# Kernel tuning notes

Measured on AMD Instinct MI355X. Metric: run time of the kernel, lower is better.

Reference implementation:

```python
import jax, jax.numpy as jnp
import numpy as np

SEQ = 8192
VOCAB = 100000
EMB = 256
HID = 4            # must equal N_QUBITS for the gate elementwise math to broadcast
N_QUBITS = 4
TAGS = 10


def _qlayer(x, p):
    """Analytic 4-qubit circuit: RX(x_w) then RX(p_w) per wire, CNOT ring, PauliZ expvals.

    Consecutive RX gates add angles: a_w = x_w + p_w; single-qubit <Z> = cos(a_w).
    CNOTs permute computational basis states, so final bit w is an XOR of the
    independent input bits along the ring, giving products of cos terms:
      <Z_0> = z1*z2*z3, <Z_1> = z0*z1, <Z_2> = z0*z1*z2, <Z_3> = z0*z1*z2*z3.
    x: [B, 4], p: [4] -> [B, 4]
    """
    z = jnp.cos(x + p)
    z0, z1, z2, z3 = z[:, 0], z[:, 1], z[:, 2], z[:, 3]
    return jnp.stack([z1 * z2 * z3, z0 * z1, z0 * z1 * z2, z0 * z1 * z2 * z3], axis=-1)


def setup_inputs() -> dict:
    key = jax.random.key(0)
    ks = jax.random.split(key, 16)
    s = 1.0 / np.sqrt(EMB + HID)
    inp = {
        "sentence": jax.random.randint(ks[0], (SEQ,), 0, VOCAB),
        "embed": jax.random.normal(ks[1], (VOCAB, EMB), dtype=jnp.float32),
        "Wf": jax.random.uniform(ks[2], (EMB + HID, N_QUBITS), minval=-s, maxval=s),
        "bf": jax.random.uniform(ks[3], (N_QUBITS,), minval=-s, maxval=s),
        "Wi": jax.random.uniform(ks[4], (EMB + HID, N_QUBITS), minval=-s, maxval=s),
        "bi": jax.random.uniform(ks[5], (N_QUBITS,), minval=-s, maxval=s),
        "Wu": jax.random.uniform(ks[6], (EMB + HID, N_QUBITS), minval=-s, maxval=s),
        "bu": jax.random.uniform(ks[7], (N_QUBITS,), minval=-s, maxval=s),
        "Wo": jax.random.uniform(ks[8], (EMB + HID, N_QUBITS), minval=-s, maxval=s),
        "bo": jax.random.uniform(ks[9], (N_QUBITS,), minval=-s, maxval=s),
        "pf": jax.random.uniform(ks[10], (N_QUBITS,), minval=0.0, maxval=2 * np.pi),
        "pi_": jax.random.uniform(ks[11], (N_QUBITS,), minval=0.0, maxval=2 * np.pi),
        "pu": jax.random.uniform(ks[12], (N_QUBITS,), minval=0.0, maxval=2 * np.pi),
        "po": jax.random.uniform(ks[13], (N_QUBITS,), minval=0.0, maxval=2 * np.pi),
        "W_tag": jax.random.uniform(ks[14], (HID, TAGS), minval=-0.5, maxval=0.5),
        "b_tag": jax.random.uniform(ks[15], (TAGS,), minval=-0.5, maxval=0.5),
    }
    return inp


def reference(sentence, embed, Wf, bf, Wi, bi, Wu, bu, Wo, bo, pf, pi_, pu, po, W_tag, b_tag):
    embeds = embed[sentence]  # [S, EMB] gather (memory-bound)

    def step(carry, x):
        hx, cx = carry  # each [1, HID]
        comb = jnp.concatenate([x[None, :], hx], axis=1)  # [1, EMB+HID]
        f = jax.nn.sigmoid(_qlayer(comb @ Wf + bf, pf))
        i = jax.nn.sigmoid(_qlayer(comb @ Wi + bi, pi_))
        g = jnp.tanh(_qlayer(comb @ Wu + bu, pu))
        o = jax.nn.sigmoid(_qlayer(comb @ Wo + bo, po))
        cx = f * cx + i * g
        hx = o * jnp.tanh(cx)
        return (hx, cx), hx[0]

    init = (jnp.zeros((1, HID), embeds.dtype), jnp.zeros((1, HID), embeds.dtype))
    _, outs = jax.lax.scan(step, init, embeds)  # outs: [S, HID]
    logits = outs @ W_tag + b_tag  # [S, TAGS]
    return jax.nn.log_softmax(logits, axis=1)
```

## Files before the change

### kernel.cpp

```cpp
#include <hip/hip_runtime.h>
#include <hip/hip_bf16.h>

#define SEQ   8192
#define EMB   256
#define TAGS  10
#define PFD   8
#define CHUNK 8
#define WARM  16

static_assert(SEQ % CHUNK == 0, "chunks tile SEQ");
static_assert(CHUNK % PFD == 0 && WARM % PFD == 0, "unroll");

constexpr float INV2PI  = 0.15915494309189535f;

#define QR1   0x39
#define QR2   0x4E
#define QR3   0x93
#define SHL4  0x104
#define SHL8  0x108
#define SHL12 0x10C
#define SHR4  0x114
#define SHR8  0x118
#define SHR12 0x11C

template<int CTRL>
__device__ __forceinline__ float fdpp(float x) {
    return __builtin_bit_cast(float,
        __builtin_amdgcn_update_dpp(0, __builtin_bit_cast(int, x),
                                    CTRL, 0xF, 0xF, true));
}

__device__ __forceinline__ float fract_f(float a) {
#if __has_builtin(__builtin_amdgcn_fractf)
    return __builtin_amdgcn_fractf(a);
#else
    return a - floorf(a);
#endif
}
__device__ __forceinline__ float cos_rev(float a) {
    float r = fract_f(a);
#if __has_builtin(__builtin_amdgcn_cosf)
    return __builtin_amdgcn_cosf(r);
#else
    return __cosf(r * 6.2831853071795864f);
#endif
}

#define K1  0.99988000f
#define K3 -0.33064200f
#define K5  0.11945370f
#define K7 -0.02727870f
#define B0  0.99958010f
#define B1 -0.32717320f
#define B2  0.11471900f
#define B3 -0.03006680f
#define B4  0.00466450f
#define B5 -0.00030650f

#define ACCQ(E, W0, W1, W2, W3) do {                                          \
    ax = fmaf((E).x, (W0).x, ax); ay = fmaf((E).x, (W0).y, ay);               \
    az = fmaf((E).x, (W0).z, az); aw = fmaf((E).x, (W0).w, aw);               \
    ax = fmaf((E).y, (W1).x, ax); ay = fmaf((E).y, (W1).y, ay);               \
    az = fmaf((E).y, (W1).z, az); aw = fmaf((E).y, (W1).w, aw);               \
    ax = fmaf((E).z, (W2).x, ax); ay = fmaf((E).z, (W2).y, ay);               \
    az = fmaf((E).z, (W2).z, az); aw = fmaf((E).z, (W2).w, aw);               \
    ax = fmaf((E).w, (W3).x, ax); ay = fmaf((E).w, (W3).y, ay);               \
    az = fmaf((E).w, (W3).z, az); aw = fmaf((E).w, (W3).w, aw);               \
} while (0)

#define LOADE(P0, P1, P2, P3, EB) do {                                        \
    P0 = *reinterpret_cast<const float4*>((EB) + 0);                          \
    P1 = *reinterpret_cast<const float4*>((EB) + 4);                          \
    P2 = *reinterpret_cast<const float4*>((EB) + 8);                          \
    P3 = *reinterpret_cast<const float4*>((EB) + 12);                         \
} while (0)

#define COMPE(P0, P1, P2, P3, T) do {                                         \
    float ax = 0.f, ay = 0.f, az = 0.f, aw = 0.f;                             \
    ACCQ(P0, Wv[0],  Wv[1],  Wv[2],  Wv[3]);                                  \
    ACCQ(P1, Wv[4],  Wv[5],  Wv[6],  Wv[7]);                                  \
    ACCQ(P2, Wv[8],  Wv[9],  Wv[10], Wv[11]);                                 \
    ACCQ(P3, Wv[12], Wv[13], Wv[14], Wv[15]);                                 \
    ax += __shfl_xor(ax, 4, 64);  ay += __shfl_xor(ay, 4, 64);                \
    az += __shfl_xor(az, 4, 64);  aw += __shfl_xor(aw, 4, 64);                \
    ax += __shfl_xor(ax, 8, 64);  ay += __shfl_xor(ay, 8, 64);                \
    az += __shfl_xor(az, 8, 64);  aw += __shfl_xor(aw, 8, 64);                \
    ax += __shfl_xor(ax, 16, 64); ay += __shfl_xor(ay, 16, 64);               \
    az += __shfl_xor(az, 16, 64); aw += __shfl_xor(aw, 16, 64);               \
    ax += __shfl_xor(ax, 32, 64); ay += __shfl_xor(ay, 32, 64);               \
    az += __shfl_xor(az, 32, 64); aw += __shfl_xor(aw, 32, 64);               \
    if (lane < 4) {                                                           \
        float4 r;                                                             \
        r.x = (ax + bp0) * INV2PI;                                            \
        r.y = (ay + bp1) * INV2PI;                                            \
        r.z = (az + bp2) * INV2PI;                                            \
        r.w = (aw + bp3) * INV2PI;                                            \
        *reinterpret_cast<float4*>(pre + (T) * 16 + g * 4) = r;               \
    }                                                                         \
} while (0)

__global__ __launch_bounds__(256) void k_pre(
    const int*   __restrict__ sentence, const float* __restrict__ embed,
    const float* __restrict__ Wf, const float* __restrict__ bf,
    const float* __restrict__ Wi, const float* __restrict__ bi,
    const float* __restrict__ Wu, const float* __restrict__ bu,
    const float* __restrict__ Wo, const float* __restrict__ bo,
    const float* __restrict__ pf, const float* __restrict__ ppi,
    const float* __restrict__ pu, const float* __restrict__ po,
    float* __restrict__ pre)
{
    const int wv   = threadIdx.x >> 6;
    const int lane = threadIdx.x & 63;
    const int g    = lane & 3;
    const int kc   = (lane >> 2) & 15;
    const int t0   = (blockIdx.x * 4 + wv) * 4;

    const float* Wg = (g == 0) ? Wf : (g == 1) ? Wi : (g == 2) ? Wu : Wo;
    const float* wb = Wg + kc * 64;

    float4 Wv[16];
#pragma unroll
    for (int i = 0; i < 16; ++i)
        Wv[i] = *reinterpret_cast<const float4*>(wb + i * 4);

    const float* bg = (g == 0) ? bf : (g == 1) ? bi : (g == 2) ? bu : bo;
    const float* pg = (g == 0) ? pf : (g == 1) ? ppi : (g == 2) ? pu : po;
    const float bp0 = bg[0] + pg[0];
    const float bp1 = bg[1] + pg[1];
    const float bp2 = bg[2] + pg[2];
    const float bp3 = bg[3] + pg[3];

    const float* e0 = embed + (long long)sentence[t0 + 0] * EMB + kc * 16;
    const float* e1 = embed + (long long)sentence[t0 + 1] * EMB + kc * 16;
    const float* e2 = embed + (long long)sentence[t0 + 2] * EMB + kc * 16;
    const float* e3 = embed + (long long)sentence[t0 + 3] * EMB + kc * 16;

    float4 A0, A1, A2, A3, Bq0, Bq1, Bq2, Bq3;
    LOADE(A0, A1, A2, A3, e0);
    LOADE(Bq0, Bq1, Bq2, Bq3, e1);
    COMPE(A0, A1, A2, A3, t0 + 0);
    LOADE(A0, A1, A2, A3, e2);
    COMPE(Bq0, Bq1, Bq2, Bq3, t0 + 1);
    LOADE(Bq0, Bq1, Bq2, Bq3, e3);
    COMPE(A0, A1, A2, A3, t0 + 2);
    COMPE(Bq0, Bq1, Bq2, Bq3, t0 + 3);
}

__global__ __launch_bounds__(64) void k_scanout(
    const float* __restrict__ pre,
    const float* __restrict__ Wf, const float* __restrict__ Wi,
    const float* __restrict__ Wu, const float* __restrict__ Wo,
    const float* __restrict__ Wt, const float* __restrict__ bt,
    float* __restrict__ out)
{
    __shared__ float sH[CHUNK * 4];

    const int lane = threadIdx.x & 15;
    const int w = lane & 3, g = lane >> 2;

    const int c       = blockIdx.x;
    const int start   = c * CHUNK;
    const int t_begin = (start >= WARM) ? (start - WARM) : 0;
    const int nsteps  = (start + CHUNK) - t_begin;

    {
        const float* Wg = (g == 0) ? Wf : (g == 1) ? Wi : (g == 2) ? Wu : Wo;
        const float c0 = Wg[(EMB + ((w + 0) & 3)) * 4 + w] * INV2PI;
        const float c1 = Wg[(EMB + ((w + 1) & 3)) * 4 + w] * INV2PI;
        const float c2 = Wg[(EMB + ((w + 2) & 3)) * 4 + w] * INV2PI;
        const float c3 = Wg[(EMB + ((w + 3) & 3)) * 4 + w] * INV2PI;

        const bool  isU = (g == 2);
        const float alp = isU ? 1.0f : 0.5f;
        const float bet = isU ? 1.0f : 0.5f;
        const float gam = isU ? 0.0f : 0.5f;

        const int smask = (w == 0) ? 0xE : (w == 1) ? 0x3 : (w == 2) ? 0x7 : 0xF;
        const bool i0 = (smask >> ((w + 0) & 3)) & 1;
        const bool i1 = (smask >> ((w + 1) & 3)) & 1;
        const bool i2 = (smask >> ((w + 2) & 3)) & 1;
        const bool i3 = (smask >> ((w + 3) & 3)) & 1;

        float buf[PFD];
#pragma unroll
        for (int d = 0; d < PFD; ++d) buf[d] = pre[(t_begin + d) * 16 + lane];

        float h0 = 0.f, h1 = 0.f, h2 = 0.f, h3 = 0.f, cx = 0.f;

        for (int s0 = 0; s0 < nsteps; s0 += PFD) {
#pragma unroll
            for (int d = 0; d < PFD; ++d) {
                const int t = t_begin + s0 + d;
                const float pv = buf[d];
                buf[d] = pre[(t + PFD) * 16 + lane];

                const float a0 = fmaf(h0, c0, pv);
                const float a1 = fmaf(h1, c1, a0);
                const float m2d = h2 * c2;
                const float a2 = fmaf(h3, c3, m2d);
                const float a  = a1 + a2;
                const float z  = cos_rev(a);

                const float z1 = fdpp<QR1>(z);
                const float z2 = fdpp<QR2>(z);
                const float z3 = fdpp<QR3>(z);
                const float m0 = i0 ? z  : 1.f;
                const float m1 = i1 ? z1 : 1.f;
                const float m2 = i2 ? z2 : 1.f;
                const float m3 = i3 ? z3 : 1.f;
                const float q  = (m0 * m1) * (m2 * m3);

                const float x   = q * alp;
                const float u   = x * x;
                const float u2p = u * u;
                const float cA  = fmaf(K7, u, K5);
                const float cB  = fmaf(K3, u, K1);
                const float dd  = fmaf(cA, u2p, cB);
                const float v   = x * dd;
                const float y   = fmaf(bet, v, gam);

                const float s4  = fdpp<SHL4 >(y);
                const float s8  = fdpp<SHL8 >(y);
                const float s12 = fdpp<SHL12>(y);
                const float r4  = fdpp<SHR4 >(y);
                const float r8  = fdpp<SHR8 >(y);
                const float r12 = fdpp<SHR12>(y);
                const float Fg = (g == 0) ? y   : (g == 1) ? r4 : (g == 2) ? r8 : r12;
                const float Ig = (g == 0) ? s4  : (g == 1) ? y  : (g == 2) ? r4 : r8;
                const float Ug = (g == 0) ? s8  : (g == 1) ? s4 : (g == 2) ? y  : r4;
                const float Og = (g == 0) ? s12 : (g == 1) ? s8 : (g == 2) ? s4 : y;

                cx = fmaf(Fg, cx, Ig * Ug);

                const float cu  = cx * cx;
                const float cu2 = cu * cu;
                const float cu4 = cu2 * cu2;
                const float e0  = fmaf(B1, cu, B0);
                const float e1  = fmaf(B3, cu, B2);
                const float e2  = fmaf(B5, cu, B4);
                const float f0  = fmaf(e1, cu2, e0);
                const float f1  = fmaf(e2, cu4, f0);
                const float th  = cx * f1;
                const float h   = Og * th;

                if (t >= start && threadIdx.x < 4) sH[(t - start) * 4 + w] = h;

                h0 = h;
                h1 = fdpp<QR1>(h);
                h2 = fdpp<QR2>(h);
                h3 = fdpp<QR3>(h);
            }
        }
    }
    __syncthreads();

    {
        const int tok = threadIdx.x >> 3;
        const int j   = threadIdx.x & 7;
        const bool has2 = (j < 2);

        const float hh0 = sH[tok * 4 + 0];
        const float hh1 = sH[tok * 4 + 1];
        const float hh2 = sH[tok * 4 + 2];
        const float hh3 = sH[tok * 4 + 3];

        float lgA = bt[j];
        lgA = fmaf(hh0, Wt[0 * TAGS + j], lgA);
        lgA = fmaf(hh1, Wt[1 * TAGS + j], lgA);
        lgA = fmaf(hh2, Wt[2 * TAGS + j], lgA);
        lgA = fmaf(hh3, Wt[3 * TAGS + j], lgA);

        const int j2 = has2 ? (j + 8) : j;
        float lgB = bt[j2];
        lgB = fmaf(hh0, Wt[0 * TAGS + j2], lgB);
        lgB = fmaf(hh1, Wt[1 * TAGS + j2], lgB);
        lgB = fmaf(hh2, Wt[2 * TAGS + j2], lgB);
        lgB = fmaf(hh3, Wt[3 * TAGS + j2], lgB);

        float vm = fmaxf(lgA, has2 ? lgB : -1e30f);
        vm = fmaxf(vm, __shfl_xor(vm, 1, 64));
        vm = fmaxf(vm, __shfl_xor(vm, 2, 64));
        vm = fmaxf(vm, __shfl_xor(vm, 4, 64));

        float e = expf(lgA - vm) + (has2 ? expf(lgB - vm) : 0.f);
        e += __shfl_xor(e, 1, 64);
        e += __shfl_xor(e, 2, 64);
        e += __shfl_xor(e, 4, 64);

        const float ls = logf(e) + vm;
        const int t = start + tok;
        out[t * TAGS + j] = lgA - ls;
        if (has2) out[t * TAGS + j + 8] = lgB - ls;
    }
}

extern "C" void kernel_launch(void* const* d_in, const int* in_sizes, int n_in,
                              void* d_out, int out_size, void* d_ws, size_t ws_size,
                              hipStream_t stream) {
    const int*   sentence = (const int*)  d_in[0];
    const float* embed    = (const float*)d_in[1];
    const float* Wf  = (const float*)d_in[2];
    const float* bf  = (const float*)d_in[3];
    const float* Wi  = (const float*)d_in[4];
    const float* bi  = (const float*)d_in[5];
    const float* Wu  = (const float*)d_in[6];
    const float* bu  = (const float*)d_in[7];
    const float* Wo  = (const float*)d_in[8];
    const float* bo  = (const float*)d_in[9];
    const float* pf  = (const float*)d_in[10];
    const float* ppi = (const float*)d_in[11];
    const float* pu  = (const float*)d_in[12];
    const float* po  = (const float*)d_in[13];
    const float* Wt  = (const float*)d_in[14];
    const float* bt  = (const float*)d_in[15];

    float* pre = (float*)d_ws;

    k_pre<<<SEQ / 16, 256, 0, stream>>>(sentence, embed, Wf, bf, Wi, bi,
                                        Wu, bu, Wo, bo, pf, ppi, pu, po, pre);
    k_scanout<<<SEQ / CHUNK, 64, 0, stream>>>(pre, Wf, Wi, Wu, Wo,
                                              Wt, bt, (float*)d_out);
}
```

Before: 18.82 us.

## Fuse projection and scan kernels, recomputing window projections per block in LDS

Merges the gate-projection kernel and the chunked scan/output kernel into one launch. Each block now gathers embeddings and computes the pre-activations for its own warm-up plus chunk window into shared memory, and wave 0 then runs the scan from LDS. This removes the second launch and the global workspace write and read. In exchange, each token's projection is computed three times (window 24 vs chunk 8), which triples embedding gather traffic and adds a serial phase before the scan in every block.

```diff
diff --git a/kernel.cpp b/kernel.cpp
--- a/kernel.cpp
+++ b/kernel.cpp
@@ -7,9 +7,13 @@
 #define PFD   8
 #define CHUNK 8
 #define WARM  16
+#define WIN   (WARM + CHUNK)
+#define NWAVE 4
+#define TPW   6
 
 static_assert(SEQ % CHUNK == 0, "chunks tile SEQ");
-static_assert(CHUNK % PFD == 0 && WARM % PFD == 0, "unroll");
+static_assert(CHUNK == PFD && WARM % PFD == 0, "unroll");
+static_assert(NWAVE * TPW == WIN, "window coverage");
 
 constexpr float INV2PI  = 0.15915494309189535f;
 
@@ -75,7 +79,7 @@
     P3 = *reinterpret_cast<const float4*>((EB) + 12);                         \
 } while (0)
 
-#define COMPE(P0, P1, P2, P3, T) do {                                         \
+#define COMPE(P0, P1, P2, P3, SLOT) do {                                      \
     float ax = 0.f, ay = 0.f, az = 0.f, aw = 0.f;                             \
     ACCQ(P0, Wv[0],  Wv[1],  Wv[2],  Wv[3]);                                  \
     ACCQ(P1, Wv[4],  Wv[5],  Wv[6],  Wv[7]);                                  \
@@ -95,11 +99,11 @@
         r.y = (ay + bp1) * INV2PI;                                            \
         r.z = (az + bp2) * INV2PI;                                            \
         r.w = (aw + bp3) * INV2PI;                                            \
-        *reinterpret_cast<float4*>(pre + (T) * 16 + g * 4) = r;               \
+        *reinterpret_cast<float4*>(sPre + (SLOT) * 16 + g * 4) = r;           \
     }                                                                         \
 } while (0)
 
-__global__ __launch_bounds__(256) void k_pre(
+__global__ __launch_bounds__(NWAVE * 64) void k_all(
     const int*   __restrict__ sentence, const float* __restrict__ embed,
     const float* __restrict__ Wf, const float* __restrict__ bf,
     const float* __restrict__ Wi, const float* __restrict__ bi,
@@ -107,63 +111,67 @@
     const float* __restrict__ Wo, const float* __restrict__ bo,
     const float* __restrict__ pf, const float* __restrict__ ppi,
     const float* __restrict__ pu, const float* __restrict__ po,
-    float* __restrict__ pre)
-{
-    const int wv   = threadIdx.x >> 6;
-    const int lane = threadIdx.x & 63;
-    const int g    = lane & 3;
-    const int kc   = (lane >> 2) & 15;
-    const int t0   = (blockIdx.x * 4 + wv) * 4;
-
-    const float* Wg = (g == 0) ? Wf : (g == 1) ? Wi : (g == 2) ? Wu : Wo;
-    const float* wb = Wg + kc * 64;
-
-    float4 Wv[16];
-#pragma unroll
-    for (int i = 0; i < 16; ++i)
-        Wv[i] = *reinterpret_cast<const float4*>(wb + i * 4);
-
-    const float* bg = (g == 0) ? bf : (g == 1) ? bi : (g == 2) ? bu : bo;
-    const float* pg = (g == 0) ? pf : (g == 1) ? ppi : (g == 2) ? pu : po;
-    const float bp0 = bg[0] + pg[0];
-    const float bp1 = bg[1] + pg[1];
-    const float bp2 = bg[2] + pg[2];
-    const float bp3 = bg[3] + pg[3];
-
-    const float* e0 = embed + (long long)sentence[t0 + 0] * EMB + kc * 16;
-    const float* e1 = embed + (long long)sentence[t0 + 1] * EMB + kc * 16;
-    const float* e2 = embed + (long long)sentence[t0 + 2] * EMB + kc * 16;
-    const float* e3 = embed + (long long)sentence[t0 + 3] * EMB + kc * 16;
-
-    float4 A0, A1, A2, A3, Bq0, Bq1, Bq2, Bq3;
-    LOADE(A0, A1, A2, A3, e0);
-    LOADE(Bq0, Bq1, Bq2, Bq3, e1);
-    COMPE(A0, A1, A2, A3, t0 + 0);
-    LOADE(A0, A1, A2, A3, e2);
-    COMPE(Bq0, Bq1, Bq2, Bq3, t0 + 1);
-    LOADE(Bq0, Bq1, Bq2, Bq3, e3);
-    COMPE(A0, A1, A2, A3, t0 + 2);
-    COMPE(Bq0, Bq1, Bq2, Bq3, t0 + 3);
-}
-
-__global__ __launch_bounds__(64) void k_scanout(
-    const float* __restrict__ pre,
-    const float* __restrict__ Wf, const float* __restrict__ Wi,
-    const float* __restrict__ Wu, const float* __restrict__ Wo,
     const float* __restrict__ Wt, const float* __restrict__ bt,
     float* __restrict__ out)
 {
+    __shared__ float sPre[(WIN + PFD) * 16];
     __shared__ float sH[CHUNK * 4];
-
-    const int lane = threadIdx.x & 15;
-    const int w = lane & 3, g = lane >> 2;
 
     const int c       = blockIdx.x;
     const int start   = c * CHUNK;
     const int t_begin = (start >= WARM) ? (start - WARM) : 0;
     const int nsteps  = (start + CHUNK) - t_begin;
 
+    const int wv   = threadIdx.x >> 6;
+    const int lane = threadIdx.x & 63;
+
     {
+        const int g  = lane & 3;
+        const int kc = (lane >> 2) & 15;
+
+        const float* Wg = (g == 0) ? Wf : (g == 1) ? Wi : (g == 2) ? Wu : Wo;
+        const float* wb = Wg + kc * 64;
+
+        float4 Wv[16];
+#pragma unroll
+        for (int i = 0; i < 16; ++i)
+            Wv[i] = *reinterpret_cast<const float4*>(wb + i * 4);
+
+        const float* bg = (g == 0) ? bf : (g == 1) ? bi : (g == 2) ? bu : bo;
+        const float* pg = (g == 0) ? pf : (g == 1) ? ppi : (g == 2) ? pu : po;
+        const float bp0 = bg[0] + pg[0];
+        const float bp1 = bg[1] + pg[1];
+        const float bp2 = bg[2] + pg[2];
+        const float bp3 = bg[3] + pg[3];
+
+        const int s0 = wv * TPW;
+        const float* e0 = embed + (long long)sentence[t_begin + s0 + 0] * EMB + kc * 16;
+        const float* e1 = embed + (long long)sentence[t_begin + s0 + 1] * EMB + kc * 16;
+        const float* e2 = embed + (long long)sentence[t_begin + s0 + 2] * EMB + kc * 16;
+        const float* e3 = embed + (long long)sentence[t_begin + s0 + 3] * EMB + kc * 16;
+        const float* e4 = embed + (long long)sentence[t_begin + s0 + 4] * EMB + kc * 16;
+        const float* e5 = embed + (long long)sentence[t_begin + s0 + 5] * EMB + kc * 16;
+
+        float4 A0, A1, A2, A3, Bq0, Bq1, Bq2, Bq3;
+        LOADE(A0, A1, A2, A3, e0);
+        LOADE(Bq0, Bq1, Bq2, Bq3, e1);
+        COMPE(A0, A1, A2, A3, s0 + 0);
+        LOADE(A0, A1, A2, A3, e2);
+        COMPE(Bq0, Bq1, Bq2, Bq3, s0 + 1);
+        LOADE(Bq0, Bq1, Bq2, Bq3, e3);
+        COMPE(A0, A1, A2, A3, s0 + 2);
+        LOADE(A0, A1, A2, A3, e4);
+        COMPE(Bq0, Bq1, Bq2, Bq3, s0 + 3);
+        LOADE(Bq0, Bq1, Bq2, Bq3, e5);
+        COMPE(A0, A1, A2, A3, s0 + 4);
+        COMPE(Bq0, Bq1, Bq2, Bq3, s0 + 5);
+    }
+    __syncthreads();
+
+    if (wv == 0) {
+        const int l16 = threadIdx.x & 15;
+        const int w = l16 & 3, g = l16 >> 2;
+
         const float* Wg = (g == 0) ? Wf : (g == 1) ? Wi : (g == 2) ? Wu : Wo;
         const float c0 = Wg[(EMB + ((w + 0) & 3)) * 4 + w] * INV2PI;
         const float c1 = Wg[(EMB + ((w + 1) & 3)) * 4 + w] * INV2PI;
@@ -183,7 +191,7 @@
 
         float buf[PFD];
 #pragma unroll
-        for (int d = 0; d < PFD; ++d) buf[d] = pre[(t_begin + d) * 16 + lane];
+        for (int d = 0; d < PFD; ++d) buf[d] = sPre[d * 16 + l16];
 
         float h0 = 0.f, h1 = 0.f, h2 = 0.f, h3 = 0.f, cx = 0.f;
 
@@ -192,7 +200,7 @@
             for (int d = 0; d < PFD; ++d) {
                 const int t = t_begin + s0 + d;
                 const float pv = buf[d];
-                buf[d] = pre[(t + PFD) * 16 + lane];
+                buf[d] = sPre[(s0 + d + PFD) * 16 + l16];
 
                 const float a0 = fmaf(h0, c0, pv);
                 const float a1 = fmaf(h1, c1, a0);
@@ -254,7 +262,7 @@
     }
     __syncthreads();
 
-    {
+    if (threadIdx.x < 64) {
         const int tok = threadIdx.x >> 3;
         const int j   = threadIdx.x & 7;
         const bool has2 = (j < 2);
@@ -314,10 +322,8 @@
     const float* Wt  = (const float*)d_in[14];
     const float* bt  = (const float*)d_in[15];
 
-    float* pre = (float*)d_ws;
-
-    k_pre<<<SEQ / 16, 256, 0, stream>>>(sentence, embed, Wf, bf, Wi, bi,
-                                        Wu, bu, Wo, bo, pf, ppi, pu, po, pre);
-    k_scanout<<<SEQ / CHUNK, 64, 0, stream>>>(pre, Wf, Wi, Wu, Wo,
-                                              Wt, bt, (float*)d_out);
-}
+    k_all<<<SEQ / CHUNK, NWAVE * 64, 0, stream>>>(sentence, embed,
+                                                  Wf, bf, Wi, bi, Wu, bu,
+                                                  Wo, bo, pf, ppi, pu, po,
+                                                  Wt, bt, (float*)d_out);
+}
```

Result: slower. 24.22 us (+28.7%).
